# Kernel tuning notes

Measured on AMD Instinct MI355X. Metric: run time of the kernel, lower is better.

## Reference

```python
import jax, jax.numpy as jnp
import numpy as np

DOF = 7
B = 8192
DT = 0.1
ACTION_RANGE = 50.0
MAX_VEL = 20.0


def _skew(w):
    x, y, z = w[..., 0], w[..., 1], w[..., 2]
    O = jnp.zeros_like(x)
    return jnp.stack([jnp.stack([O, -z, y], -1),
                      jnp.stack([z, O, -x], -1),
                      jnp.stack([-y, x, O], -1)], -2)


def _exp_se3(xi):
    # xi: (..., 6) twist [w; v] (already scaled by joint angle) -> (..., 4, 4)
    w, v = xi[..., :3], xi[..., 3:]
    th = jnp.sqrt(jnp.sum(w * w, -1))
    small = th < 1e-4
    ths = jnp.where(small, 1.0, th)  # safe denominator
    th2 = th * th
    a = jnp.where(small, 1.0 - th2 / 6.0, jnp.sin(th) / ths)
    b = jnp.where(small, 0.5 - th2 / 24.0, (1.0 - jnp.cos(th)) / (ths * ths))
    c = jnp.where(small, 1.0 / 6.0 - th2 / 120.0, (th - jnp.sin(th)) / (ths * ths * ths))
    K = _skew(w)
    K2 = K @ K
    I3 = jnp.eye(3, dtype=xi.dtype)
    R = I3 + a[..., None, None] * K + b[..., None, None] * K2
    Vm = I3 + b[..., None, None] * K + c[..., None, None] * K2
    p = jnp.einsum('...ij,...j->...i', Vm, v)
    top = jnp.concatenate([R, p[..., None]], -1)
    bot = jnp.broadcast_to(jnp.array([0.0, 0.0, 0.0, 1.0], xi.dtype), top.shape[:-2] + (1, 4))
    return jnp.concatenate([top, bot], -2)


def _inv_T(T):
    R = T[..., :3, :3]
    p = T[..., :3, 3]
    Rt = jnp.swapaxes(R, -1, -2)
    pn = -jnp.einsum('...ij,...j->...i', Rt, p)
    top = jnp.concatenate([Rt, pn[..., None]], -1)
    bot = jnp.broadcast_to(jnp.array([0.0, 0.0, 0.0, 1.0], T.dtype), top.shape[:-2] + (1, 4))
    return jnp.concatenate([top, bot], -2)


def _adjoint(T):
    # SE(3) adjoint for [w; v] twists: [[R, 0], [ [p]x R, R ]]
    R = T[..., :3, :3]
    p = T[..., :3, 3]
    pR = _skew(p) @ R
    Z = jnp.zeros_like(R)
    return jnp.concatenate([jnp.concatenate([R, Z], -1),
                            jnp.concatenate([pR, R], -1)], -2)


def _ad(V):
    # se(3) little adjoint: [[ [w]x, 0 ], [ [v]x, [w]x ]]
    Kw = _skew(V[..., :3])
    Kv = _skew(V[..., 3:])
    Z = jnp.zeros_like(Kw)
    return jnp.concatenate([jnp.concatenate([Kw, Z], -1),
                            jnp.concatenate([Kv, Kw], -1)], -2)


def _inverse_dynamics(q, dq, ddq, g, Ftip, M, G, A):
    # Recursive Newton-Euler (Modern Robotics, link-frame screws A).
    Bq, n = q.shape
    V = jnp.zeros((Bq, 6), q.dtype)
    Vd = jnp.broadcast_to(jnp.concatenate([jnp.zeros(3, q.dtype), -g]), (Bq, 6))
    AdTs, Vs, Vds = [], [], []
    for i in range(n):
        T = _exp_se3(-A[i] * q[:, i, None]) @ _inv_T(M[i])  # T_{i,i-1}, (B,4,4)
        AdT = _adjoint(T)
        V = jnp.einsum('bij,bj->bi', AdT, V) + A[i] * dq[:, i, None]
        Vd = (jnp.einsum('bij,bj->bi', AdT, Vd)
              + jnp.einsum('bij,j->bi', _ad(V), A[i]) * dq[:, i, None]
              + A[i] * ddq[:, i, None])
        AdTs.append(AdT)
        Vs.append(V)
        Vds.append(Vd)
    F = jnp.broadcast_to(Ftip.astype(q.dtype), (Bq, 6))
    AdT_end = _adjoint(_inv_T(M[n]))  # T_{n+1,n}, (6,6)
    taus = [None] * n
    for i in range(n - 1, -1, -1):
        if i == n - 1:
            F = jnp.einsum('ji,bj->bi', AdT_end, F)
        else:
            F = jnp.einsum('bji,bj->bi', AdTs[i + 1], F)
        F = (F + jnp.einsum('ij,bj->bi', G[i], Vds[i])
             - jnp.einsum('bji,jk,bk->bi', _ad(Vs[i]), G[i], Vs[i]))
        taus[i] = jnp.einsum('bi,i->b', F, A[i])
    return jnp.stack(taus, -1)  # (B, n)


def _forward_dynamics(q, dq, tau, g, Ftip, M, G, A):
    n = q.shape[1]
    zer = jnp.zeros_like(q)
    # bias forces: Coriolis + gravity + end-effector wrench
    h = _inverse_dynamics(q, dq, zer, g, Ftip, M, G, A)
    g0 = jnp.zeros(3, q.dtype)
    f0 = jnp.zeros(6, q.dtype)
    # mass matrix columns via unit accelerations (vmapped over columns)
    cols = jax.vmap(lambda e: _inverse_dynamics(
        q, zer, jnp.broadcast_to(e, q.shape), g0, f0, M, G, A))(jnp.eye(n, dtype=q.dtype))
    Mmat = jnp.transpose(cols, (1, 2, 0))  # (B, n, n)
    return jnp.linalg.solve(Mmat, (tau - h)[..., None])[..., 0]


def _fk_in_space(q, M, A):
    Bq, n = q.shape
    T = jnp.broadcast_to(jnp.eye(4, dtype=q.dtype), (Bq, 4, 4))
    outs = []
    for i in range(n):
        T = (T @ M[i]) @ _exp_se3(A[i] * q[:, i, None])
        outs.append(T)
    outs.append(T @ M[n])
    return jnp.stack(outs, 1)  # (B, n+1, 4, 4)


def setup_inputs():
    key = jax.random.key(0)
    ks = jax.random.split(key, 4)
    state = jax.random.normal(ks[0], (B, 2 * DOF), jnp.float32)
    torque = jax.random.normal(ks[1], (B, DOF), jnp.float32)
    M = jnp.tile(jnp.eye(4, dtype=jnp.float32)[None], (DOF + 1, 1, 1))
    A = jax.random.uniform(ks[2], (DOF, 6), jnp.float32)
    L = jax.random.normal(ks[3], (DOF, 6, 6), jnp.float32)
    gravity = jnp.array([0.0, -9.8, 0.0], jnp.float32)
    ftip = jnp.zeros(6, jnp.float32)
    return {"state": state, "torque": torque, "M": M, "A": A, "L": L,
            "gravity": gravity, "ftip": ftip}


def reference(state, torque, M, A, L, gravity, ftip):
    n = DOF
    G = L @ jnp.swapaxes(L, -1, -2)  # spatial inertias, PSD
    s0 = jnp.concatenate([state, torque * ACTION_RANGE], -1)  # (B, 3n)

    def derivs(s):
        q = s[..., :n]
        dq = s[..., n:2 * n]
        qf = s[..., 2 * n:]
        qacc = _forward_dynamics(q, dq, qf, gravity, ftip, M, G, A)
        return jnp.concatenate([dq, qacc, jnp.zeros_like(qf)], -1)

    k1 = derivs(s0)
    k2 = derivs(s0 + 0.5 * DT * k1)
    k3 = derivs(s0 + 0.5 * DT * k2)
    k4 = derivs(s0 + DT * k3)
    s1 = s0 + (DT / 6.0) * (k1 + 2.0 * k2 + 2.0 * k3 + k4)
    q = jnp.mod(s1[..., :n] + jnp.pi, 2.0 * jnp.pi) - jnp.pi
    dq = jnp.clip(s1[..., n:2 * n], -MAX_VEL, MAX_VEL)
    ee = _fk_in_space(q, M, A)
    return jnp.concatenate([q, dq], -1), ee[:, -1, :2, 3]
```

## Files before the change

kernel.cpp:

```cpp
#include <hip/hip_runtime.h>
#include <hip/hip_bf16.h>

#define DTC 0.1f
#define ACTION_RANGE 50.0f
#define MAX_VEL 20.0f
#define PI_F 3.14159265358979323846f
#define TWO_PI_F 6.28318530717958647692f
#define INV_TWO_PI_F 0.15915494309189533577f

__device__ __forceinline__ float bf2f(__hip_bfloat16 x){ return __bfloat162float(x); }

__device__ __forceinline__ float ldv(const void* p, int i, bool isb){
  return isb ? __bfloat162float(((const __hip_bfloat16*)p)[i]) : ((const float*)p)[i];
}
__device__ __forceinline__ void stv(void* p, int i, float v, bool isb){
  if (isb) ((__hip_bfloat16*)p)[i] = __float2bfloat16(v);
  else     ((float*)p)[i] = v;
}

__device__ __forceinline__ void exp_se3_Rp(const float* Aj, float s, float* R, float* P){
  float wx=Aj[0]*s, wy=Aj[1]*s, wz=Aj[2]*s;
  float vx=Aj[3]*s, vy=Aj[4]*s, vz=Aj[5]*s;
  float th2 = wx*wx+wy*wy+wz*wz;
  float th = sqrtf(th2);
  float a,b,c;
  if (th < 0.25f){
    float th4 = th2*th2;
    a = 1.f - th2*(1.f/6.f) + th4*(1.f/120.f);
    b = 0.5f - th2*(1.f/24.f) + th4*(1.f/720.f);
    c = (1.f/6.f) - th2*(1.f/120.f) + th4*(1.f/5040.f);
  } else {
    float sn = sinf(th), cs = cosf(th);
    float inv = 1.f/th, inv2 = inv*inv;
    a = sn*inv;
    b = (1.f-cs)*inv2;
    c = (th-sn)*inv2*inv;
  }
  R[0]=1.f+b*(wx*wx-th2); R[1]=b*wx*wy-a*wz;      R[2]=b*wx*wz+a*wy;
  R[3]=b*wx*wy+a*wz;      R[4]=1.f+b*(wy*wy-th2); R[5]=b*wy*wz-a*wx;
  R[6]=b*wx*wz-a*wy;      R[7]=b*wy*wz+a*wx;      R[8]=1.f+b*(wz*wz-th2);
  float V0=1.f+c*(wx*wx-th2), V1=c*wx*wy-b*wz,      V2=c*wx*wz+b*wy;
  float V3=c*wx*wy+b*wz,      V4=1.f+c*(wy*wy-th2), V5=c*wy*wz-b*wx;
  float V6=c*wx*wz-b*wy,      V7=c*wy*wz+b*wx,      V8=1.f+c*(wz*wz-th2);
  P[0]=V0*vx+V1*vy+V2*vz;
  P[1]=V3*vx+V4*vy+V5*vz;
  P[2]=V6*vx+V7*vy+V8*vz;
}

__device__ __forceinline__ void mul33(const float* X, const float* Y, float* Z){
  #pragma unroll
  for (int r=0;r<3;r++){
    float x0=X[r*3+0], x1=X[r*3+1], x2=X[r*3+2];
    Z[r*3+0]=x0*Y[0]+x1*Y[3]+x2*Y[6];
    Z[r*3+1]=x0*Y[1]+x1*Y[4]+x2*Y[7];
    Z[r*3+2]=x0*Y[2]+x1*Y[5]+x2*Y[8];
  }
}

__device__ __forceinline__ void ad_apply(const float* R, const float* p, const float* Vin, float* Vout){
  float i0=Vin[0],i1=Vin[1],i2=Vin[2],i3=Vin[3],i4=Vin[4],i5=Vin[5];
  float w0 = R[0]*i0+R[1]*i1+R[2]*i2;
  float w1 = R[3]*i0+R[4]*i1+R[5]*i2;
  float w2 = R[6]*i0+R[7]*i1+R[8]*i2;
  float r0 = R[0]*i3+R[1]*i4+R[2]*i5;
  float r1 = R[3]*i3+R[4]*i4+R[5]*i5;
  float r2 = R[6]*i3+R[7]*i4+R[8]*i5;
  float p0=p[0],p1=p[1],p2=p[2];
  Vout[0]=w0; Vout[1]=w1; Vout[2]=w2;
  Vout[3]=p1*w2-p2*w1+r0;
  Vout[4]=p2*w0-p0*w2+r1;
  Vout[5]=p0*w1-p1*w0+r2;
}

__device__ __forceinline__ void adT_apply(const float* R, const float* p, const float* Fin, float* Fout){
  float m0=Fin[0],m1=Fin[1],m2=Fin[2],f0=Fin[3],f1=Fin[4],f2=Fin[5];
  float p0=p[0],p1=p[1],p2=p[2];
  float cx = m0 - (p1*f2 - p2*f1);
  float cy = m1 - (p2*f0 - p0*f2);
  float cz = m2 - (p0*f1 - p1*f0);
  float o0 = R[0]*cx + R[3]*cy + R[6]*cz;
  float o1 = R[1]*cx + R[4]*cy + R[7]*cz;
  float o2 = R[2]*cx + R[5]*cy + R[8]*cz;
  float o3 = R[0]*f0 + R[3]*f1 + R[6]*f2;
  float o4 = R[1]*f0 + R[4]*f1 + R[7]*f2;
  float o5 = R[2]*f0 + R[5]*f1 + R[8]*f2;
  Fout[0]=o0;Fout[1]=o1;Fout[2]=o2;Fout[3]=o3;Fout[4]=o4;Fout[5]=o5;
}

__device__ __forceinline__ void gmatvec(const float* G, const float* v, float* out){
  float v0=v[0],v1=v[1],v2=v[2],v3=v[3],v4=v[4],v5=v[5];
  #pragma unroll
  for (int r=0;r<6;r++)
    out[r] = G[r*6+0]*v0+G[r*6+1]*v1+G[r*6+2]*v2+G[r*6+3]*v3+G[r*6+4]*v4+G[r*6+5]*v5;
}

#define W_STRIDE 97

__global__ __launch_bounds__(64) void arm_rk4_kernel(
    const void* __restrict__ g_state,
    const void* __restrict__ g_torque,
    const void* __restrict__ g_M,
    const void* __restrict__ g_A,
    const void* __restrict__ g_L,
    const void* __restrict__ g_grav,
    const void* __restrict__ g_ftip,
    void* __restrict__ g_out,
    int B)
{
  __shared__ float sA[42];
  __shared__ float sG[252];
  __shared__ float sMinvR[72];
  __shared__ float sMinvp[24];
  __shared__ float sMR[72];
  __shared__ float sMp[24];
  __shared__ float sgrav[3];
  __shared__ float sftip[6];
  __shared__ float sW[8*W_STRIDE];

  const bool isb = fabsf(bf2f(((const __hip_bfloat16*)g_grav)[1]) + 9.8f) < 0.5f;

  const int t = threadIdx.x;
  for (int x=t; x<42; x+=64) sA[x] = ldv(g_A, x, isb);
  for (int x=t; x<252; x+=64){
    int i = x/36; int rc = x - i*36; int rr = rc/6; int cc = rc - rr*6;
    float s = 0.f;
    #pragma unroll
    for (int k=0;k<6;k++) s += ldv(g_L, i*36+rr*6+k, isb) * ldv(g_L, i*36+cc*6+k, isb);
    sG[x] = s;
  }
  if (t < 8){
    float R[9], p[3];
    #pragma unroll
    for (int rr=0;rr<3;rr++){
      #pragma unroll
      for (int cc=0;cc<3;cc++) R[rr*3+cc] = ldv(g_M, t*16 + rr*4 + cc, isb);
      p[rr] = ldv(g_M, t*16 + rr*4 + 3, isb);
    }
    #pragma unroll
    for (int rr=0;rr<3;rr++){
      #pragma unroll
      for (int cc=0;cc<3;cc++){ sMR[t*9+rr*3+cc] = R[rr*3+cc]; sMinvR[t*9+rr*3+cc] = R[cc*3+rr]; }
      sMp[t*3+rr] = p[rr];
      sMinvp[t*3+rr] = -(R[0*3+rr]*p[0] + R[1*3+rr]*p[1] + R[2*3+rr]*p[2]);
    }
  }
  if (t == 0){ for (int k=0;k<3;k++) sgrav[k] = ldv(g_grav, k, isb); }
  if (t == 1){ for (int k=0;k<6;k++) sftip[k] = ldv(g_ftip, k, isb); }
  __syncthreads();

  const int e = t >> 3;
  const int r = t & 7;
  int b = blockIdx.x * 8 + e;
  if (b >= B) b = B - 1;
  const bool is7 = (r == 7);
  float* W = &sW[e*W_STRIDE];

  float q0[7], dq0[7], qf[7];
  #pragma unroll
  for (int i=0;i<7;i++){
    q0[i]  = ldv(g_state, b*14+i, isb);
    dq0[i] = ldv(g_state, b*14+7+i, isb);
    qf[i]  = ldv(g_torque, b*7+i, isb) * ACTION_RANGE;
  }
  float kq[7], kdd[7], accq[7], accdq[7];
  #pragma unroll
  for (int i=0;i<7;i++){ kq[i]=0.f; kdd[i]=0.f; accq[i]=0.f; accdq[i]=0.f; }

  float Fend[6];
  {
    float tf[6]; adT_apply(&sMinvR[63], &sMinvp[21], sftip, tf);
    #pragma unroll
    for (int k=0;k<6;k++) Fend[k] = is7 ? tf[k] : 0.f;
  }

  #pragma unroll 1
  for (int st=0; st<4; ++st){
    const float cin = (st==0) ? 0.f : ((st==3) ? DTC : 0.5f*DTC);
    const float wgt = (st==0||st==3) ? (DTC/6.f) : (DTC/3.f);
    float qs[7], dqs[7];
    #pragma unroll
    for (int i=0;i<7;i++){ qs[i]=q0[i]+cin*kq[i]; dqs[i]=dq0[i]+cin*kdd[i]; }

    float qsr = 0.f;
    #pragma unroll
    for (int c=0;c<7;c++) qsr = (r==c) ? qs[c] : qsr;

    if (r < 7){
      float Re[9], Pe[3], Rt[9];
      exp_se3_Rp(&sA[r*6], -qsr, Re, Pe);
      mul33(Re, &sMinvR[r*9], Rt);
      #pragma unroll
      for (int k=0;k<9;k++) W[r*12+k] = Rt[k];
      #pragma unroll
      for (int rr=0;rr<3;rr++)
        W[r*12+9+rr] = Re[rr*3+0]*sMinvp[r*3+0] + Re[rr*3+1]*sMinvp[r*3+1]
                     + Re[rr*3+2]*sMinvp[r*3+2] + Pe[rr];
    }
    __syncthreads();

    float Va[7][6], Vda[7][6];
    float V[6] = {0,0,0,0,0,0};
    float Vd[6];
    Vd[0]=0.f; Vd[1]=0.f; Vd[2]=0.f;
    Vd[3] = is7 ? -sgrav[0] : 0.f;
    Vd[4] = is7 ? -sgrav[1] : 0.f;
    Vd[5] = is7 ? -sgrav[2] : 0.f;
    #pragma unroll
    for (int i=0;i<7;i++){
      const float* R = &W[i*12];
      const float* p = R+9;
      float dqi  = is7 ? dqs[i] : 0.f;
      float ddqi = is7 ? 0.f : ((r==i) ? 1.f : 0.f);
      ad_apply(R,p,V,V);
      #pragma unroll
      for (int k=0;k<6;k++) V[k] += sA[i*6+k]*dqi;
      ad_apply(R,p,Vd,Vd);
      {
        float w0=V[0],w1=V[1],w2=V[2],v0=V[3],v1=V[4],v2=V[5];
        float a0=sA[i*6+0],a1=sA[i*6+1],a2=sA[i*6+2],a3=sA[i*6+3],a4=sA[i*6+4],a5=sA[i*6+5];
        Vd[0] += (w1*a2-w2*a1)*dqi + a0*ddqi;
        Vd[1] += (w2*a0-w0*a2)*dqi + a1*ddqi;
        Vd[2] += (w0*a1-w1*a0)*dqi + a2*ddqi;
        Vd[3] += ((v1*a2-v2*a1)+(w1*a5-w2*a4))*dqi + a3*ddqi;
        Vd[4] += ((v2*a0-v0*a2)+(w2*a3-w0*a5))*dqi + a4*ddqi;
        Vd[5] += ((v0*a1-v1*a0)+(w0*a4-w1*a3))*dqi + a5*ddqi;
      }
      #pragma unroll
      for (int k=0;k<6;k++){ Va[i][k]=V[k]; Vda[i][k]=Vd[k]; }
    }

    float m[7];
    {
      float F[6];
      #pragma unroll
      for (int k=0;k<6;k++) F[k] = Fend[k];
      #pragma unroll
      for (int i=6;i>=0;i--){
        if (i<6) adT_apply(&W[(i+1)*12], &W[(i+1)*12+9], F, F);
        float gv[6], gvd[6];
        gmatvec(&sG[i*36], Va[i], gv);
        gmatvec(&sG[i*36], Vda[i], gvd);
        float w0=Va[i][0],w1=Va[i][1],w2=Va[i][2],v0=Va[i][3],v1=Va[i][4],v2=Va[i][5];
        F[0] += gvd[0] + (w1*gv[2]-w2*gv[1]) + (v1*gv[5]-v2*gv[4]);
        F[1] += gvd[1] + (w2*gv[0]-w0*gv[2]) + (v2*gv[3]-v0*gv[5]);
        F[2] += gvd[2] + (w0*gv[1]-w1*gv[0]) + (v0*gv[4]-v1*gv[3]);
        F[3] += gvd[3] + (w1*gv[5]-w2*gv[4]);
        F[4] += gvd[4] + (w2*gv[3]-w0*gv[5]);
        F[5] += gvd[5] + (w0*gv[4]-w1*gv[3]);
        m[i] = F[0]*sA[i*6+0]+F[1]*sA[i*6+1]+F[2]*sA[i*6+2]
             + F[3]*sA[i*6+3]+F[4]*sA[i*6+4]+F[5]*sA[i*6+5];
      }
    }

    float rhs = 0.f;
    #pragma unroll
    for (int c=0;c<7;c++){
      float hc = __shfl(m[c], 7, 8);
      rhs = (r==c) ? (qf[c]-hc) : rhs;
    }
    #pragma unroll
    for (int k=0;k<7;k++){
      float pvk   = __shfl(m[k], k, 8);
      float pvrhs = __shfl(rhs,  k, 8);
      float pinv  = 1.f/pvk;
      float f = (r>k) ? m[k]*pinv : 0.f;
      #pragma unroll
      for (int c=k+1;c<7;c++){
        float pvc = __shfl(m[c], k, 8);
        m[c] -= f*pvc;
      }
      rhs -= f*pvrhs;
    }
    float x[7];
    #pragma unroll
    for (int i=6;i>=0;i--){
      float di = __shfl(m[i], i, 8);
      float si = __shfl(rhs, i, 8);
      float xi = si/di;
      x[i] = xi;
      rhs -= ((r<i) ? m[i] : 0.f) * xi;
    }

    #pragma unroll
    for (int i=0;i<7;i++){
      kq[i]  = dqs[i];
      kdd[i] = x[i];
      accq[i]  += wgt*dqs[i];
      accdq[i] += wgt*x[i];
    }
    __syncthreads();
  }

  float q1r=0.f, dq1r=0.f;
  #pragma unroll
  for (int c=0;c<7;c++){
    float xx = q0[c] + accq[c] + PI_F;
    float mm = xx - floorf(xx * INV_TWO_PI_F) * TWO_PI_F;
    float qv = mm - PI_F;
    float dv = dq0[c] + accdq[c];
    dv = fminf(fmaxf(dv, -MAX_VEL), MAX_VEL);
    q1r  = (r==c) ? qv : q1r;
    dq1r = (r==c) ? dv : dq1r;
  }

  {
    float XR[9], Xp[3];
    if (r < 7){
      float Re[9], Pe[3];
      exp_se3_Rp(&sA[r*6], q1r, Re, Pe);
      mul33(&sMR[r*9], Re, XR);
      #pragma unroll
      for (int rr=0;rr<3;rr++)
        Xp[rr] = sMR[r*9+rr*3+0]*Pe[0]+sMR[r*9+rr*3+1]*Pe[1]+sMR[r*9+rr*3+2]*Pe[2] + sMp[r*3+rr];
    } else {
      #pragma unroll
      for (int k=0;k<9;k++) XR[k] = sMR[63+k];
      #pragma unroll
      for (int k=0;k<3;k++) Xp[k] = sMp[21+k];
    }
    #pragma unroll
    for (int k=0;k<9;k++) W[r*12+k]   = XR[k];
    #pragma unroll
    for (int k=0;k<3;k++) W[r*12+9+k] = Xp[k];
  }
  __syncthreads();

  #pragma unroll
  for (int w=4; w>=1; w>>=1){
    float Ra[9], pa[3], Rb[9], pb[3];
    if (r < w){
      #pragma unroll
      for (int k=0;k<9;k++){ Ra[k]=W[(2*r)*12+k]; Rb[k]=W[(2*r+1)*12+k]; }
      #pragma unroll
      for (int k=0;k<3;k++){ pa[k]=W[(2*r)*12+9+k]; pb[k]=W[(2*r+1)*12+9+k]; }
    }
    __syncthreads();
    if (r < w){
      float Rc[9];
      mul33(Ra, Rb, Rc);
      #pragma unroll
      for (int k=0;k<9;k++) W[r*12+k] = Rc[k];
      #pragma unroll
      for (int rr=0;rr<3;rr++)
        W[r*12+9+rr] = Ra[rr*3+0]*pb[0]+Ra[rr*3+1]*pb[1]+Ra[rr*3+2]*pb[2] + pa[rr];
    }
    __syncthreads();
  }

  if (r < 7){
    stv(g_out, b*14+r,   q1r,  isb);
    stv(g_out, b*14+7+r, dq1r, isb);
  } else {
    stv(g_out, B*14 + b*2 + 0, W[9],  isb);
    stv(g_out, B*14 + b*2 + 1, W[10], isb);
  }
}

extern "C" void kernel_launch(void* const* d_in, const int* in_sizes, int n_in,
                              void* d_out, int out_size, void* d_ws, size_t ws_size,
                              hipStream_t stream) {
  const int B = in_sizes[0] / 14;
  const int blocks = (B + 7) / 8;
  arm_rk4_kernel<<<blocks, 64, 0, stream>>>(d_in[0], d_in[1], d_in[2], d_in[3],
                                            d_in[4], d_in[5], d_in[6], d_out, B);
}
```

Measured before the change: 95.05 us.

## Cache screw axes in registers, use fast intrinsics, and solve mass matrix per-lane

Loads the joint screw axes and inverse home-frame transforms from shared memory into registers once, so the RNEA loops no longer read shared memory repeatedly. The exp map now computes both branches and selects with fast __sinf/__cosf and hardware reciprocal instead of branching. The 7x7 mass-matrix solve changes from a shuffle-heavy distributed elimination to broadcasting the upper triangle to every lane, which then does a redundant symmetric Gaussian elimination in registers. The kernel also gains launch_bounds(64,1). The trade-off is much higher register pressure and lower-precision transcendentals and reciprocals.

```diff
diff --git a/kernel.cpp b/kernel.cpp
--- a/kernel.cpp
+++ b/kernel.cpp
@@ -9,6 +9,7 @@
 #define INV_TWO_PI_F 0.15915494309189533577f
 
 __device__ __forceinline__ float bf2f(__hip_bfloat16 x){ return __bfloat162float(x); }
+__device__ __forceinline__ float frcp(float x){ return __builtin_amdgcn_rcpf(x); }
 
 __device__ __forceinline__ float ldv(const void* p, int i, bool isb){
   return isb ? __bfloat162float(((const __hip_bfloat16*)p)[i]) : ((const float*)p)[i];
@@ -23,19 +24,17 @@
   float vx=Aj[3]*s, vy=Aj[4]*s, vz=Aj[5]*s;
   float th2 = wx*wx+wy*wy+wz*wz;
   float th = sqrtf(th2);
-  float a,b,c;
-  if (th < 0.25f){
-    float th4 = th2*th2;
-    a = 1.f - th2*(1.f/6.f) + th4*(1.f/120.f);
-    b = 0.5f - th2*(1.f/24.f) + th4*(1.f/720.f);
-    c = (1.f/6.f) - th2*(1.f/120.f) + th4*(1.f/5040.f);
-  } else {
-    float sn = sinf(th), cs = cosf(th);
-    float inv = 1.f/th, inv2 = inv*inv;
-    a = sn*inv;
-    b = (1.f-cs)*inv2;
-    c = (th-sn)*inv2*inv;
-  }
+  float th4 = th2*th2;
+  float aS = 1.f - th2*(1.f/6.f)  + th4*(1.f/120.f);
+  float bS = 0.5f - th2*(1.f/24.f) + th4*(1.f/720.f);
+  float cS = (1.f/6.f) - th2*(1.f/120.f) + th4*(1.f/5040.f);
+  float sn = __sinf(th), cs = __cosf(th);
+  float inv = frcp(th), inv2 = inv*inv;
+  float aL = sn*inv;
+  float bL = (1.f-cs)*inv2;
+  float cL = (th-sn)*inv2*inv;
+  bool sm = th < 0.25f;
+  float a = sm?aS:aL, b = sm?bS:bL, c = sm?cS:cL;
   R[0]=1.f+b*(wx*wx-th2); R[1]=b*wx*wy-a*wz;      R[2]=b*wx*wz+a*wy;
   R[3]=b*wx*wy+a*wz;      R[4]=1.f+b*(wy*wy-th2); R[5]=b*wy*wz-a*wx;
   R[6]=b*wx*wz-a*wy;      R[7]=b*wy*wz+a*wx;      R[8]=1.f+b*(wz*wz-th2);
@@ -96,7 +95,7 @@
 
 #define W_STRIDE 97
 
-__global__ __launch_bounds__(64) void arm_rk4_kernel(
+__global__ __launch_bounds__(64, 1) void arm_rk4_kernel(
     const void* __restrict__ g_state,
     const void* __restrict__ g_torque,
     const void* __restrict__ g_M,
@@ -155,6 +154,25 @@
   const bool is7 = (r == 7);
   float* W = &sW[e*W_STRIDE];
 
+  float Areg[7][6];
+  #pragma unroll
+  for (int i=0;i<7;i++)
+    #pragma unroll
+    for (int k=0;k<6;k++) Areg[i][k] = sA[i*6+k];
+  float Aown[6];
+  #pragma unroll
+  for (int k=0;k<6;k++){
+    float v = 0.f;
+    #pragma unroll
+    for (int c=0;c<7;c++) v = (r==c) ? Areg[c][k] : v;
+    Aown[k] = v;
+  }
+  float MiR[9], Mip[3];
+  #pragma unroll
+  for (int k=0;k<9;k++) MiR[k] = sMinvR[r*9+k];
+  #pragma unroll
+  for (int k=0;k<3;k++) Mip[k] = sMinvp[r*3+k];
+
   float q0[7], dq0[7], qf[7];
   #pragma unroll
   for (int i=0;i<7;i++){
@@ -187,14 +205,14 @@
 
     if (r < 7){
       float Re[9], Pe[3], Rt[9];
-      exp_se3_Rp(&sA[r*6], -qsr, Re, Pe);
-      mul33(Re, &sMinvR[r*9], Rt);
+      exp_se3_Rp(Aown, -qsr, Re, Pe);
+      mul33(Re, MiR, Rt);
       #pragma unroll
       for (int k=0;k<9;k++) W[r*12+k] = Rt[k];
       #pragma unroll
       for (int rr=0;rr<3;rr++)
-        W[r*12+9+rr] = Re[rr*3+0]*sMinvp[r*3+0] + Re[rr*3+1]*sMinvp[r*3+1]
-                     + Re[rr*3+2]*sMinvp[r*3+2] + Pe[rr];
+        W[r*12+9+rr] = Re[rr*3+0]*Mip[0] + Re[rr*3+1]*Mip[1]
+                     + Re[rr*3+2]*Mip[2] + Pe[rr];
     }
     __syncthreads();
 
@@ -213,11 +231,11 @@
       float ddqi = is7 ? 0.f : ((r==i) ? 1.f : 0.f);
       ad_apply(R,p,V,V);
       #pragma unroll
-      for (int k=0;k<6;k++) V[k] += sA[i*6+k]*dqi;
+      for (int k=0;k<6;k++) V[k] += Areg[i][k]*dqi;
       ad_apply(R,p,Vd,Vd);
       {
         float w0=V[0],w1=V[1],w2=V[2],v0=V[3],v1=V[4],v2=V[5];
-        float a0=sA[i*6+0],a1=sA[i*6+1],a2=sA[i*6+2],a3=sA[i*6+3],a4=sA[i*6+4],a5=sA[i*6+5];
+        float a0=Areg[i][0],a1=Areg[i][1],a2=Areg[i][2],a3=Areg[i][3],a4=Areg[i][4],a5=Areg[i][5];
         Vd[0] += (w1*a2-w2*a1)*dqi + a0*ddqi;
         Vd[1] += (w2*a0-w0*a2)*dqi + a1*ddqi;
         Vd[2] += (w0*a1-w1*a0)*dqi + a2*ddqi;
@@ -247,38 +265,38 @@
         F[3] += gvd[3] + (w1*gv[5]-w2*gv[4]);
         F[4] += gvd[4] + (w2*gv[3]-w0*gv[5]);
         F[5] += gvd[5] + (w0*gv[4]-w1*gv[3]);
-        m[i] = F[0]*sA[i*6+0]+F[1]*sA[i*6+1]+F[2]*sA[i*6+2]
-             + F[3]*sA[i*6+3]+F[4]*sA[i*6+4]+F[5]*sA[i*6+5];
+        m[i] = F[0]*Areg[i][0]+F[1]*Areg[i][1]+F[2]*Areg[i][2]
+             + F[3]*Areg[i][3]+F[4]*Areg[i][4]+F[5]*Areg[i][5];
       }
     }
 
-    float rhs = 0.f;
-    #pragma unroll
-    for (int c=0;c<7;c++){
-      float hc = __shfl(m[c], 7, 8);
-      rhs = (r==c) ? (qf[c]-hc) : rhs;
-    }
+    float U[7][7];
+    #pragma unroll
+    for (int i=0;i<7;i++){
+      #pragma unroll
+      for (int j=i;j<7;j++) U[i][j] = __shfl(m[j], i, 8);
+    }
+    float rv[7];
+    #pragma unroll
+    for (int i=0;i<7;i++) rv[i] = qf[i] - __shfl(m[i], 7, 8);
     #pragma unroll
     for (int k=0;k<7;k++){
-      float pvk   = __shfl(m[k], k, 8);
-      float pvrhs = __shfl(rhs,  k, 8);
-      float pinv  = 1.f/pvk;
-      float f = (r>k) ? m[k]*pinv : 0.f;
-      #pragma unroll
-      for (int c=k+1;c<7;c++){
-        float pvc = __shfl(m[c], k, 8);
-        m[c] -= f*pvc;
+      float dinv = frcp(U[k][k]);
+      #pragma unroll
+      for (int i=k+1;i<7;i++){
+        float f = U[k][i]*dinv;
+        #pragma unroll
+        for (int j=i;j<7;j++) U[i][j] -= f*U[k][j];
+        rv[i] -= f*rv[k];
       }
-      rhs -= f*pvrhs;
     }
     float x[7];
     #pragma unroll
     for (int i=6;i>=0;i--){
-      float di = __shfl(m[i], i, 8);
-      float si = __shfl(rhs, i, 8);
-      float xi = si/di;
-      x[i] = xi;
-      rhs -= ((r<i) ? m[i] : 0.f) * xi;
+      float s = rv[i];
+      #pragma unroll
+      for (int j=i+1;j<7;j++) s -= U[i][j]*x[j];
+      x[i] = s*frcp(U[i][i]);
     }
 
     #pragma unroll
@@ -307,7 +325,7 @@
     float XR[9], Xp[3];
     if (r < 7){
       float Re[9], Pe[3];
-      exp_se3_Rp(&sA[r*6], q1r, Re, Pe);
+      exp_se3_Rp(Aown, q1r, Re, Pe);
       mul33(&sMR[r*9], Re, XR);
       #pragma unroll
       for (int rr=0;rr<3;rr++)
```

Result: slower. 177.3 us (+86.5%).
